# Performance work log

Hardware: AMD Instinct MI355X
Metric: run time of the kernel (lower is better)

The kernel has to match this reference:

```python
import jax, jax.numpy as jnp
import numpy as np

B, N, D, H, T, DFF, OUT = 32, 256, 512, 8, 60, 2048, 2
EPS = 1e-5


def _mha(q, k, v, Wq, Wk, Wv, Wo, bq, bk, bv, bo):
    # torch nn.MultiheadAttention (batch_first): x @ W.T + b projections
    Bq, Lq, Dm = q.shape
    dh = Dm // H
    scale = 1.0 / np.sqrt(dh).astype(np.float32)
    qh = (q @ Wq.T + bq).reshape(Bq, Lq, H, dh).transpose(0, 2, 1, 3)
    kh = (k @ Wk.T + bk).reshape(Bq, k.shape[1], H, dh).transpose(0, 2, 1, 3)
    vh = (v @ Wv.T + bv).reshape(Bq, v.shape[1], H, dh).transpose(0, 2, 1, 3)
    a = jax.nn.softmax(jnp.einsum('bhqd,bhkd->bhqk', qh, kh) * scale, axis=-1)
    o = jnp.einsum('bhqk,bhkd->bhqd', a, vh).transpose(0, 2, 1, 3).reshape(Bq, Lq, Dm)
    return o @ Wo.T + bo


def _ln(x, w, b):
    m = x.mean(-1, keepdims=True)
    v = ((x - m) ** 2).mean(-1, keepdims=True)
    return (x - m) / jnp.sqrt(v + EPS) * w + b


def setup_inputs() -> dict:
    key = jax.random.key(0)
    ks = iter(jax.random.split(key, 64))

    def rn(shape, s=0.05):
        return jax.random.normal(next(ks), shape, dtype=jnp.float32) * s

    inp = {
        'H_v_all': rn((B, N, D), 1.0),
        'H_v0_init': rn((B, 1, 1, D), 1.0),
        'pe': rn((1, T, D), 1.0),  # positional_encoding parameter
    }
    # s_* : spatial_attn;  sa_* : decoder self-attn;  ca_* : decoder cross-attn
    for p in ('s', 'sa', 'ca'):
        for m in ('Wq', 'Wk', 'Wv', 'Wo'):
            inp[f'{p}_{m}'] = rn((D, D))
        for m in ('bq', 'bk', 'bv', 'bo'):
            inp[f'{p}_{m}'] = jnp.zeros((D,), jnp.float32)
    for i in (1, 2, 3):
        inp[f'ln{i}_w'] = jnp.ones((D,), jnp.float32)
        inp[f'ln{i}_b'] = jnp.zeros((D,), jnp.float32)
    inp['W1'] = rn((DFF, D)); inp['b1'] = jnp.zeros((DFF,), jnp.float32)
    inp['W2'] = rn((D, DFF)); inp['b2'] = jnp.zeros((D,), jnp.float32)
    inp['Wout'] = rn((OUT, D)); inp['bout'] = jnp.zeros((OUT,), jnp.float32)
    return inp


def reference(H_v_all, H_v0_init, pe,
              s_Wq, s_Wk, s_Wv, s_Wo, s_bq, s_bk, s_bv, s_bo,
              sa_Wq, sa_Wk, sa_Wv, sa_Wo, sa_bq, sa_bk, sa_bv, sa_bo,
              ca_Wq, ca_Wk, ca_Wv, ca_Wo, ca_bq, ca_bk, ca_bv, ca_bo,
              ln1_w, ln1_b, ln2_w, ln2_b, ln3_w, ln3_b,
              W1, b1, W2, b2, Wout, bout):

    def dec_layer(x, mem):
        # post-norm TransformerDecoderLayer, no masks (non-causal), relu FFN, eval (no dropout)
        sa = _mha(x, x, x, sa_Wq, sa_Wk, sa_Wv, sa_Wo, sa_bq, sa_bk, sa_bv, sa_bo)
        x = _ln(x + sa, ln1_w, ln1_b)
        ca = _mha(x, mem, mem, ca_Wq, ca_Wk, ca_Wv, ca_Wo, ca_bq, ca_bk, ca_bv, ca_bo)
        x = _ln(x + ca, ln2_w, ln2_b)
        ff = jax.nn.relu(x @ W1.T + b1) @ W2.T + b2
        return _ln(x + ff, ln3_w, ln3_b)

    tgt = H_v0_init  # (B, 1, 1, D), grows along dim 2
    outputs = []
    for t in range(T):
        tgt_pe = tgt + pe[:, :t + 1][:, None]        # (B,1,t+1,D)
        tgt_step = tgt_pe.reshape(B, t + 1, D)
        ctx = _mha(tgt_step[:, -1:, :], H_v_all, H_v_all,
                   s_Wq, s_Wk, s_Wv, s_Wo, s_bq, s_bk, s_bv, s_bo)
        decoded = dec_layer(tgt_step, H_v_all)
        nxt = decoded[:, -1:, :] + ctx               # (B,1,D)
        tgt = jnp.concatenate([tgt, nxt[:, None]], axis=2)
        outputs.append(nxt[:, None])                 # (B,1,1,D)
    out_seq = jnp.concatenate(outputs, axis=2)       # (B,1,T,D)
    return out_seq @ Wout.T + bout                   # (B,1,T,2)
```

## Files before the change

kernel.cpp:

```cpp
#include <hip/hip_runtime.h>


#define NB 32
#define NN 256
#define DD 512
#define NH 8
#define DH 64
#define TT 60
#define DF 2048
#define NBLK 256
#define NTHR 512

typedef unsigned short ushort_t;
typedef _Float16 half2v __attribute__((ext_vector_type(2)));

constexpr size_t SZ_KV  = (size_t)NB * NN * DD;
constexpr size_t SZ_ROW = (size_t)NB * DD;
constexpr size_t SZ_PAR = (size_t)NB * NH * DD;
constexpr size_t OFF_KS32 = 0;
constexpr size_t OFF_VS32 = SZ_KV;
constexpr size_t OFF_KC32 = 2 * SZ_KV;
constexpr size_t OFF_VC32 = 3 * SZ_KV;
constexpr size_t OFF_X    = 0;
constexpr size_t OFF_U1P  = OFF_X   + SZ_ROW;
constexpr size_t OFF_U2P  = OFF_U1P + SZ_PAR;
constexpr size_t OFF_U3P  = OFF_U2P + SZ_PAR;
constexpr size_t OFF_CTP0 = OFF_U3P + SZ_PAR;
constexpr size_t OFF_CTP1 = OFF_CTP0 + SZ_PAR;
constexpr size_t OFF_BF   = 4 * SZ_KV;
constexpr size_t UOFF_KST = 0;
constexpr size_t UOFF_KCT = SZ_KV;
constexpr size_t UOFF_VSH = 2 * SZ_KV;
constexpr size_t UOFF_VCH = 3 * SZ_KV;
constexpr size_t UOFF_W8  = 4 * SZ_KV;
constexpr size_t UOFF_W1  = UOFF_W8 + 8ull * DD * DD;
constexpr size_t UOFF_W2  = UOFF_W1 + (size_t)DD * DF;
constexpr size_t UEND     = UOFF_W2 + (size_t)DF * DD;
constexpr size_t OFF_FLG  = OFF_BF + (UEND + 1) / 2;

constexpr unsigned DYN_LDS = 131072;

__device__ __forceinline__ float ldg_a(const float* p) {
  return __hip_atomic_load(p, __ATOMIC_RELAXED, __HIP_MEMORY_SCOPE_AGENT);
}
__device__ __forceinline__ void stg_a(float* p, float v) {
  __hip_atomic_store(p, v, __ATOMIC_RELAXED, __HIP_MEMORY_SCOPE_AGENT);
}
__device__ __forceinline__ unsigned f2pk(float a, float b) {
  return __builtin_bit_cast(unsigned, __builtin_amdgcn_cvt_pkrtz(a, b));
}
__device__ __forceinline__ ushort_t f2h(float a) {
  return (ushort_t)(f2pk(a, 0.f) & 0xffffu);
}
__device__ __forceinline__ float h2f(ushort_t u) {
  return (float)__builtin_bit_cast(_Float16, u);
}
__device__ __forceinline__ float fdot2u(unsigned a, unsigned b, float c) {
  return __builtin_amdgcn_fdot2(__builtin_bit_cast(half2v, a),
                                __builtin_bit_cast(half2v, b), c, false);
}

struct Params {
  const float *pe;
  const float *sa_bq, *sa_bk, *sa_bv, *s_bq, *sa_bo, *s_bo, *ca_bq, *ca_bo;
  const float *ln1w, *ln1b, *ln2w, *ln2b, *ln3w, *ln3b;
  const float *b1, *b2, *Wout, *bout;
  const ushort_t *w8, *w1b, *w2b;
  const ushort_t *KsT, *KcT, *VsH, *VcH;
  float *xcur, *u1p, *u2p, *u3p, *ctp0, *ctp1;
  float *out;
  unsigned *flags;
};

__device__ __forceinline__ void gbar(unsigned* fl, int tid, int h,
                                     unsigned& rnd) {
  __builtin_amdgcn_s_waitcnt(0);
  __syncthreads();
  rnd++;
  if (tid < 64) {
    if (tid == h)
      __hip_atomic_store(&fl[h], rnd, __ATOMIC_RELAXED,
                         __HIP_MEMORY_SCOPE_AGENT);
    bool wait = true;
    while (wait) {
      unsigned v = rnd;
      if (tid < 8)
        v = __hip_atomic_load(&fl[tid], __ATOMIC_RELAXED,
                              __HIP_MEMORY_SCOPE_AGENT);
      wait = __any(v < rnd);
    }
  }
  __syncthreads();
}

__global__ __launch_bounds__(512) void decode_persistent(Params P) {
  __shared__ __align__(16) float sX[2048];
  __shared__ __align__(16) float sPart[512];
  __shared__ float sAux[64];
  __shared__ __align__(16) unsigned xh[256];
  __shared__ __align__(16) unsigned ph[384];
  __shared__ __align__(16) ushort_t cacheK[TT * 78];
  __shared__ __align__(16) ushort_t cacheV[TT * 64];
  extern __shared__ __align__(16) unsigned dynLds[];
  unsigned* Ks_l = dynLds;
  unsigned* Kc_l = dynLds + 8192;
  ushort_t* Vs_l = (ushort_t*)(dynLds + 16384);
  ushort_t* Vc_l = Vs_l + 16384;

  int tid = threadIdx.x;
  int bid = blockIdx.x;
  int b = bid >> 3, h = bid & 7;
  int idx8 = bid;
  unsigned* fl = P.flags + b * 64;
  unsigned rnd = 0;

  {
    const uint4* gks = (const uint4*)((const unsigned*)P.KsT +
                       (((size_t)b * DD + h * DH) >> 1) * NN);
    const uint4* gkc = (const uint4*)((const unsigned*)P.KcT +
                       (((size_t)b * DD + h * DH) >> 1) * NN);
    const uint4* gvs = (const uint4*)(P.VsH + (size_t)idx8 * NN * DH);
    const uint4* gvc = (const uint4*)(P.VcH + (size_t)idx8 * NN * DH);
    uint4* dks = (uint4*)Ks_l;
    uint4* dkc = (uint4*)Kc_l;
    uint4* dvs = (uint4*)Vs_l;
    uint4* dvc = (uint4*)Vc_l;
    #pragma unroll
    for (int i = 0; i < 4; i++) {
      int idx = i * NTHR + tid;
      dks[idx] = gks[idx];
      dkc[idx] = gkc[idx];
      dvs[idx] = gvs[idx];
      dvc[idx] = gvc[idx];
    }
  }

  float x_f = ldg_a(P.xcur + (size_t)b * DD + tid);
  {
    float px = __shfl_xor(x_f, 1);
    if (!(tid & 1)) xh[tid >> 1] = f2pk(x_f, px);
  }
  __syncthreads();

  for (int t = 0; t < TT; t++) {
    {
      {
        int w = tid >> 6, c = tid & 63, m = w >> 1, half = w & 1;
        int col = h * DH + c;
        const uint2* wp = (const uint2*)(P.w8 + (size_t)m * DD * DD) + col;
        float acc = 0.f;
        #pragma unroll 8
        for (int kq = half * 64; kq < half * 64 + 64; kq++) {
          uint2 wv = wp[(size_t)kq * DD];
          uint2 xv = *(const uint2*)&xh[kq * 2];
          acc = fdot2u(wv.x, xv.x, acc);
          acc = fdot2u(wv.y, xv.y, acc);
        }
        sPart[tid] = acc;
      }
      __syncthreads();
      if (tid < 256) {
        int m = tid >> 6, c = tid & 63, col = h * DH + c;
        const float* bias = (m == 0) ? P.sa_bq : (m == 1) ? P.sa_bk
                          : (m == 2) ? P.sa_bv : P.s_bq;
        float val = sPart[(2 * m) * 64 + c] + sPart[(2 * m + 1) * 64 + c]
                    + bias[col];
        sX[512 + tid] = val;
        if (m == 1) cacheK[t * 78 + c] = f2h(val);
        if (m == 2) cacheV[t * 64 + c] = f2h(val);
      }
      __syncthreads();

      int L = t + 1;
      float* sQ  = sX + 512;
      float* sQs = sX + 704;
      float* sPb = sX + 768;
      if (tid < 64) {
        float e = 0.f;
        if (tid < L) {
          const unsigned* kl = (const unsigned*)(cacheK + (size_t)tid * 78);
          float a = 0.f;
          #pragma unroll 8
          for (int i = 0; i < 32; i++) {
            unsigned w = kl[i];
            a += sQ[2 * i] * h2f((ushort_t)(w & 0xffffu)) +
                 sQ[2 * i + 1] * h2f((ushort_t)(w >> 16));
          }
          e = __expf(a * 0.125f);
        }
        float s2 = e;
        #pragma unroll
        for (int s = 32; s >= 1; s >>= 1) s2 += __shfl_xor(s2, s);
        sPb[tid] = e * (1.f / s2);
        float o = 0.f;
        for (int j = 0; j < L; j++)
          o += sPb[j] * h2f(cacheV[j * 64 + tid]);
        float po = __shfl_xor(o, 1);
        if (!(tid & 1)) ph[32 + (tid >> 1)] = f2pk(o, po);
      } else if (tid < 320) {
        int n = tid - 64;
        float a = 0.f;
        #pragma unroll 8
        for (int i = 0; i < 32; i++) {
          unsigned w = Ks_l[i * NN + n];
          a += sQs[2 * i] * h2f((ushort_t)(w & 0xffffu)) +
               sQs[2 * i + 1] * h2f((ushort_t)(w >> 16));
        }
        sPart[n] = a * 0.125f;
      }
      __syncthreads();
      float* sPr = sX + 1536;
      if (tid < 256) {
        float e = __expf(sPart[tid]);
        sPr[tid] = e;
        int w = tid >> 6;
        float s2 = e;
        #pragma unroll
        for (int s = 32; s >= 1; s >>= 1) s2 += __shfl_xor(s2, s);
        if ((tid & 63) == 0) sAux[4 + w] = s2;
      }
      __syncthreads();
      float* sB = sX + 1024;
      {
        int g = tid >> 6, d = tid & 63;
        float inv = 1.f / (sAux[4] + sAux[5] + sAux[6] + sAux[7]);
        const ushort_t* vp = Vs_l + (g * 32) * DH + d;
        float acc = 0.f;
        #pragma unroll 4
        for (int n = 0; n < 32; n++) acc += sPr[g * 32 + n] * h2f(vp[n * DH]);
        sB[tid] = acc * inv;
      }
      __syncthreads();
      if (tid < 64) {
        float o = 0.f;
        #pragma unroll
        for (int i = 0; i < 8; i++) o += sB[i * 64 + tid];
        float po = __shfl_xor(o, 1);
        if (!(tid & 1)) ph[64 + (tid >> 1)] = f2pk(o, po);
      }
      __syncthreads();
      {
        float* ctp = ((t & 1) ? P.ctp1 : P.ctp0) + ((size_t)b * NH + h) * DD;
        float* u1p = P.u1p + ((size_t)b * NH + h) * DD;
        const uint2* wpa = (const uint2*)(P.w8 + 4ull * DD * DD) + tid;
        const uint2* wpb = (const uint2*)(P.w8 + 5ull * DD * DD) + tid;
        float acc1 = (h == 0) ? P.sa_bo[tid] + x_f : 0.f;
        float acc2 = (h == 0) ? P.s_bo[tid] : 0.f;
        #pragma unroll 8
        for (int j = 0; j < 16; j++) {
          int k4 = h * 16 + j;
          uint2 wv = wpa[(size_t)k4 * DD];
          uint2 x1 = *(const uint2*)&ph[32 + 2 * j];
          acc1 = fdot2u(wv.x, x1.x, acc1);
          acc1 = fdot2u(wv.y, x1.y, acc1);
          uint2 wv2 = wpb[(size_t)k4 * DD];
          uint2 x2 = *(const uint2*)&ph[64 + 2 * j];
          acc2 = fdot2u(wv2.x, x2.x, acc2);
          acc2 = fdot2u(wv2.y, x2.y, acc2);
        }
        stg_a(&u1p[tid], acc1);
        stg_a(&ctp[tid], acc2);
      }
    }
    gbar(fl, tid, h, rnd);

    float y1f;
    {
      float u = 0.f;
      {
        const float* pp = P.u1p + (size_t)b * NH * DD + tid;
        #pragma unroll
        for (int i = 0; i < 8; i++) u += ldg_a(pp + i * DD);
      }
      {
        int w = tid >> 6;
        float s = u, q2 = u * u;
        #pragma unroll
        for (int m = 32; m >= 1; m >>= 1) { s += __shfl_xor(s, m); q2 += __shfl_xor(q2, m); }
        if ((tid & 63) == 0) { sAux[w] = s; sAux[8 + w] = q2; }
      }
      __syncthreads();
      {
        float ss = 0.f, qq = 0.f;
        #pragma unroll
        for (int i = 0; i < 8; i++) { ss += sAux[i]; qq += sAux[8 + i]; }
        float mean = ss * (1.f / 512.f);
        float inv = rsqrtf(qq * (1.f / 512.f) - mean * mean + 1e-5f);
        y1f = (u - mean) * inv * P.ln1w[tid] + P.ln1b[tid];
        float py = __shfl_xor(y1f, 1);
        if (!(tid & 1)) ph[128 + (tid >> 1)] = f2pk(y1f, py);
      }
      __syncthreads();
      {
        int c = tid & 63, w = tid >> 6, col = h * DH + c;
        const uint2* wp = (const uint2*)(P.w8 + 6ull * DD * DD) + col;
        float acc = 0.f;
        #pragma unroll 8
        for (int kq = w * 16; kq < w * 16 + 16; kq++) {
          uint2 wv = wp[(size_t)kq * DD];
          uint2 xv = *(const uint2*)&ph[128 + 2 * kq];
          acc = fdot2u(wv.x, xv.x, acc);
          acc = fdot2u(wv.y, xv.y, acc);
        }
        sPart[tid] = acc;
      }
      __syncthreads();
      if (tid < 64) {
        float o = 0.f;
        #pragma unroll
        for (int i = 0; i < 8; i++) o += sPart[i * 64 + tid];
        o += P.ca_bq[h * DH + tid];
        float po = __shfl_xor(o, 1);
        if (!(tid & 1)) ph[tid >> 1] = f2pk(o, po);
      }
      __syncthreads();
      {
        int n = tid & 255, dh2 = tid >> 8;
        float a = 0.f;
        #pragma unroll 8
        for (int dw = dh2 * 16; dw < dh2 * 16 + 16; dw++)
          a = fdot2u(Kc_l[dw * NN + n], ph[dw], a);
        sPart[tid] = a;
      }
      __syncthreads();
      float* sPr = sX + 1536;
      if (tid < 256) {
        float e = __expf((sPart[tid] + sPart[256 + tid]) * 0.125f);
        sPr[tid] = e;
        int w = tid >> 6;
        float s2 = e;
        #pragma unroll
        for (int s = 32; s >= 1; s >>= 1) s2 += __shfl_xor(s2, s);
        if ((tid & 63) == 0) sAux[4 + w] = s2;
      }
      __syncthreads();
      float* sB = sX + 1024;
      {
        int g = tid >> 6, d = tid & 63;
        float inv = 1.f / (sAux[4] + sAux[5] + sAux[6] + sAux[7]);
        const ushort_t* vp = Vc_l + (g * 32) * DH + d;
        float acc = 0.f;
        #pragma unroll 4
        for (int n = 0; n < 32; n++) acc += sPr[g * 32 + n] * h2f(vp[n * DH]);
        sB[tid] = acc * inv;
      }
      __syncthreads();
      if (tid < 64) {
        float o = 0.f;
        #pragma unroll
        for (int i = 0; i < 8; i++) o += sB[i * 64 + tid];
        float po = __shfl_xor(o, 1);
        if (!(tid & 1)) ph[32 + (tid >> 1)] = f2pk(o, po);
      }
      __syncthreads();
      {
        const uint2* wp = (const uint2*)(P.w8 + 7ull * DD * DD) + tid;
        float acc = (h == 0) ? P.ca_bo[tid] + y1f : 0.f;
        #pragma unroll 8
        for (int j = 0; j < 16; j++) {
          int k4 = h * 16 + j;
          uint2 wv = wp[(size_t)k4 * DD];
          uint2 xv = *(const uint2*)&ph[32 + 2 * j];
          acc = fdot2u(wv.x, xv.x, acc);
          acc = fdot2u(wv.y, xv.y, acc);
        }
        stg_a(&P.u2p[((size_t)b * NH + h) * DD + tid], acc);
      }
    }
    gbar(fl, tid, h, rnd);

    float zf;
    {
      float v = 0.f;
      {
        const float* pp = P.u2p + (size_t)b * NH * DD + tid;
        #pragma unroll
        for (int i = 0; i < 8; i++) v += ldg_a(pp + i * DD);
      }
      {
        int w = tid >> 6;
        float s = v, q2 = v * v;
        #pragma unroll
        for (int m = 32; m >= 1; m >>= 1) { s += __shfl_xor(s, m); q2 += __shfl_xor(q2, m); }
        if ((tid & 63) == 0) { sAux[w] = s; sAux[8 + w] = q2; }
      }
      __syncthreads();
      {
        float ss = 0.f, qq = 0.f;
        #pragma unroll
        for (int i = 0; i < 8; i++) { ss += sAux[i]; qq += sAux[8 + i]; }
        float mean = ss * (1.f / 512.f);
        float inv = rsqrtf(qq * (1.f / 512.f) - mean * mean + 1e-5f);
        zf = (v - mean) * inv * P.ln2w[tid] + P.ln2b[tid];
        float pz = __shfl_xor(zf, 1);
        if (!(tid & 1)) ph[128 + (tid >> 1)] = f2pk(zf, pz);
      }
      __syncthreads();
      {
        int c = tid & 255, half = tid >> 8, col = h * 256 + c;
        const uint2* wp = (const uint2*)P.w1b + col;
        float acc = 0.f;
        #pragma unroll 8
        for (int kq = half * 64; kq < half * 64 + 64; kq++) {
          uint2 wv = wp[(size_t)kq * DF];
          uint2 xv = *(const uint2*)&ph[128 + 2 * kq];
          acc = fdot2u(wv.x, xv.x, acc);
          acc = fdot2u(wv.y, xv.y, acc);
        }
        sPart[tid] = acc;
      }
      __syncthreads();
      if (tid < 256) {
        float hv = fmaxf(sPart[tid] + sPart[256 + tid] + P.b1[h * 256 + tid], 0.f);
        float pv = __shfl_xor(hv, 1);
        if (!(tid & 1)) ph[tid >> 1] = f2pk(hv, pv);
      }
      __syncthreads();
      {
        const uint2* wp = (const uint2*)P.w2b + tid;
        float acc = (h == 0) ? zf + P.b2[tid] : 0.f;
        #pragma unroll 8
        for (int j = 0; j < 64; j++) {
          int k4 = h * 64 + j;
          uint2 wv = wp[(size_t)k4 * DD];
          uint2 xv = *(const uint2*)&ph[2 * j];
          acc = fdot2u(wv.x, xv.x, acc);
          acc = fdot2u(wv.y, xv.y, acc);
        }
        stg_a(&P.u3p[((size_t)b * NH + h) * DD + tid], acc);
      }
    }
    gbar(fl, tid, h, rnd);

    {
      float u = 0.f, ctxv = 0.f;
      {
        const float* pp = P.u3p + (size_t)b * NH * DD + tid;
        const float* cp = ((t & 1) ? P.ctp1 : P.ctp0) + (size_t)b * NH * DD + tid;
        #pragma unroll
        for (int i = 0; i < 8; i++) { u += ldg_a(pp + i * DD); ctxv += ldg_a(cp + i * DD); }
      }
      {
        int w = tid >> 6;
        float s = u, q2 = u * u;
        #pragma unroll
        for (int m = 32; m >= 1; m >>= 1) { s += __shfl_xor(s, m); q2 += __shfl_xor(q2, m); }
        if ((tid & 63) == 0) { sAux[w] = s; sAux[8 + w] = q2; }
      }
      __syncthreads();
      float ss = 0.f, qq = 0.f;
      #pragma unroll
      for (int i = 0; i < 8; i++) { ss += sAux[i]; qq += sAux[8 + i]; }
      float mean = ss * (1.f / 512.f);
      float inv = rsqrtf(qq * (1.f / 512.f) - mean * mean + 1e-5f);
      float nxt = (u - mean) * inv * P.ln3w[tid] + P.ln3b[tid] + ctxv;
      float p = (t < TT - 1) ? P.pe[(size_t)(t + 1) * DD + tid] : 0.f;
      x_f = nxt + p;
      {
        float px = __shfl_xor(x_f, 1);
        if (!(tid & 1)) xh[tid >> 1] = f2pk(x_f, px);
      }
      if (h == 0) sX[tid] = nxt;
      __syncthreads();
      if (h == 0) {
        {
          int c = tid >> 8, l = tid & 255;
          float a = sX[l] * P.Wout[(size_t)c * DD + l] +
                    sX[l + 256] * P.Wout[(size_t)c * DD + l + 256];
          #pragma unroll
          for (int m = 32; m >= 1; m >>= 1) a += __shfl_xor(a, m);
          if ((tid & 63) == 0) sAux[16 + (tid >> 6)] = a;
        }
        __syncthreads();
        if (tid == 0)
          P.out[((size_t)b * TT + t) * 2 + 0] =
              sAux[16] + sAux[17] + sAux[18] + sAux[19] + P.bout[0];
        if (tid == 256)
          P.out[((size_t)b * TT + t) * 2 + 1] =
              sAux[20] + sAux[21] + sAux[22] + sAux[23] + P.bout[1];
      }
      __syncthreads();
    }
  }
}

__global__ __launch_bounds__(256) void gemm_kv(
    const float* __restrict__ A,
    const float* __restrict__ W0, const float* __restrict__ W1_,
    const float* __restrict__ W2_, const float* __restrict__ W3_,
    const float* __restrict__ b0, const float* __restrict__ b1_,
    const float* __restrict__ b2_, const float* __restrict__ b3_,
    float* __restrict__ O0, float* __restrict__ O1,
    float* __restrict__ O2, float* __restrict__ O3) {
  __shared__ __align__(16) float As[8][128];
  __shared__ __align__(16) float Bs[8][128];
  int tid = threadIdx.x;
  int bx = blockIdx.x, by = blockIdx.y;
  int mm = bx >> 2;
  int col0 = (bx & 3) * 128;
  const float* W = mm == 0 ? W0 : mm == 1 ? W1_ : mm == 2 ? W2_ : W3_;
  const float* bias = mm == 0 ? b0 : mm == 1 ? b1_ : mm == 2 ? b2_ : b3_;
  float* O = mm == 0 ? O0 : mm == 1 ? O1 : mm == 2 ? O2 : O3;
  int tx = tid & 15, ty = tid >> 4;
  int m0 = by * 128;
  int lr = tid >> 1, lk = (tid & 1) * 4;
  const float* Ap = A + (size_t)(m0 + lr) * DD + lk;
  const float* Wp = W + (size_t)(col0 + lr) * DD + lk;
  float c[8][8] = {};
  for (int k0 = 0; k0 < DD; k0 += 8) {
    float4 av = *(const float4*)(Ap + k0);
    float4 wv = *(const float4*)(Wp + k0);
    __syncthreads();
    As[lk + 0][lr] = av.x; As[lk + 1][lr] = av.y; As[lk + 2][lr] = av.z; As[lk + 3][lr] = av.w;
    Bs[lk + 0][lr] = wv.x; Bs[lk + 1][lr] = wv.y; Bs[lk + 2][lr] = wv.z; Bs[lk + 3][lr] = wv.w;
    __syncthreads();
    #pragma unroll
    for (int k = 0; k < 8; k++) {
      float a[8], bb[8];
      *(float4*)&a[0] = *(const float4*)&As[k][ty * 8];
      *(float4*)&a[4] = *(const float4*)&As[k][ty * 8 + 4];
      *(float4*)&bb[0] = *(const float4*)&Bs[k][tx * 8];
      *(float4*)&bb[4] = *(const float4*)&Bs[k][tx * 8 + 4];
      #pragma unroll
      for (int i = 0; i < 8; i++)
        #pragma unroll
        for (int j = 0; j < 8; j++) c[i][j] += a[i] * bb[j];
    }
  }
  const float* bp = bias + col0 + tx * 8;
  for (int i = 0; i < 8; i++) {
    int row = m0 + ty * 8 + i;
    float* op = O + (size_t)row * DD + col0 + tx * 8;
    #pragma unroll
    for (int jq = 0; jq < 8; jq += 4) {
      float4 v;
      v.x = c[i][jq + 0] + bp[jq + 0];
      v.y = c[i][jq + 1] + bp[jq + 1];
      v.z = c[i][jq + 2] + bp[jq + 2];
      v.w = c[i][jq + 3] + bp[jq + 3];
      *(float4*)(op + jq) = v;
    }
  }
}

__global__ __launch_bounds__(256) void pack_kT(const float* __restrict__ Ks32,
                                               const float* __restrict__ Kc32,
                                               ushort_t* __restrict__ KsT,
                                               ushort_t* __restrict__ KcT) {
  int z = blockIdx.z;
  int b = z >> 1;
  const float* in = ((z & 1) ? Kc32 : Ks32) + (size_t)b * NN * DD;
  ushort_t* out = ((z & 1) ? KcT : KsT) + (size_t)b * NN * DD;
  int r0 = blockIdx.x * 32, c0 = blockIdx.y * 32;
  __shared__ float tile[32][33];
  int tid = threadIdx.x;
  int i = tid >> 3, j4 = (tid & 7) * 4;
  float4 v = *(const float4*)(in + (size_t)(r0 + i) * DD + c0 + j4);
  tile[i][j4] = v.x; tile[i][j4 + 1] = v.y; tile[i][j4 + 2] = v.z; tile[i][j4 + 3] = v.w;
  __syncthreads();
  int d = c0 + i;
  ushort_t* op = out + (size_t)(d >> 1) * (2 * NN) + 2 * (r0 + j4) + (d & 1);
  op[0] = f2h(tile[j4][i]);     op[2] = f2h(tile[j4 + 1][i]);
  op[4] = f2h(tile[j4 + 2][i]); op[6] = f2h(tile[j4 + 3][i]);
}

__global__ __launch_bounds__(256) void pack_vh(const float* __restrict__ Vs32,
                                               const float* __restrict__ Vc32,
                                               ushort_t* __restrict__ VsH,
                                               ushort_t* __restrict__ VcH) {
  const float* src = blockIdx.y ? Vc32 : Vs32;
  ushort_t* dst = blockIdx.y ? VcH : VsH;
  size_t idx = (size_t)blockIdx.x * 1024 + threadIdx.x * 4;
  float4 v = *(const float4*)(src + idx);
  int d512 = (int)(idx & 511);
  int n = (int)((idx >> 9) & 255);
  int b = (int)(idx >> 17);
  int h = d512 >> 6, d = d512 & 63;
  ushort_t* op = dst + (((size_t)(b * 8 + h) * NN + n) * DH + d);
  op[0] = f2h(v.x); op[1] = f2h(v.y); op[2] = f2h(v.z); op[3] = f2h(v.w);
}

struct PWItem { const float* in; ushort_t* out; int C; int K; };
struct PWArgs { PWItem m[10]; };
__global__ __launch_bounds__(256) void pack_w(PWArgs a) {
  PWItem it = a.m[blockIdx.y];
  int total = it.C * (it.K >> 2);
  int e = blockIdx.x * 256 + threadIdx.x;
  if (e >= total) return;
  int kd = it.K >> 2;
  int k4 = e % kd, col = e / kd;
  float4 v = *(const float4*)(it.in + (size_t)col * it.K + k4 * 4);
  unsigned lo = f2pk(v.x, v.y), hi = f2pk(v.z, v.w);
  ushort4 o;
  o.x = (ushort_t)(lo & 0xffffu); o.y = (ushort_t)(lo >> 16);
  o.z = (ushort_t)(hi & 0xffffu); o.w = (ushort_t)(hi >> 16);
  *((ushort4*)it.out + (size_t)k4 * it.C + col) = o;
}

__global__ __launch_bounds__(256) void init_x(const float* __restrict__ hv0,
                                              const float* __restrict__ pe,
                                              float* __restrict__ ws,
                                              unsigned* __restrict__ flags) {
  int i = blockIdx.x * 256 + threadIdx.x;
  ws[OFF_X + i] = hv0[i] + pe[i & (DD - 1)];
  if (i < 2048) flags[i] = 0u;
}

extern "C" void kernel_launch(void* const* d_in, const int* in_sizes, int n_in,
                              void* d_out, int out_size, void* d_ws, size_t ws_size,
                              hipStream_t stream) {
  const float* H_v_all = (const float*)d_in[0];
  const float* H_v0    = (const float*)d_in[1];
  const float* pe      = (const float*)d_in[2];
  const float* s_Wq = (const float*)d_in[3];
  const float* s_Wk = (const float*)d_in[4];
  const float* s_Wv = (const float*)d_in[5];
  const float* s_Wo = (const float*)d_in[6];
  const float* s_bq = (const float*)d_in[7];
  const float* s_bk = (const float*)d_in[8];
  const float* s_bv = (const float*)d_in[9];
  const float* s_bo = (const float*)d_in[10];
  const float* sa_Wq = (const float*)d_in[11];
  const float* sa_Wk = (const float*)d_in[12];
  const float* sa_Wv = (const float*)d_in[13];
  const float* sa_Wo = (const float*)d_in[14];
  const float* sa_bq = (const float*)d_in[15];
  const float* sa_bk = (const float*)d_in[16];
  const float* sa_bv = (const float*)d_in[17];
  const float* sa_bo = (const float*)d_in[18];
  const float* ca_Wq = (const float*)d_in[19];
  const float* ca_Wk = (const float*)d_in[20];
  const float* ca_Wv = (const float*)d_in[21];
  const float* ca_Wo = (const float*)d_in[22];
  const float* ca_bq = (const float*)d_in[23];
  const float* ca_bk = (const float*)d_in[24];
  const float* ca_bv = (const float*)d_in[25];
  const float* ca_bo = (const float*)d_in[26];
  const float* ln1w = (const float*)d_in[27];
  const float* ln1b = (const float*)d_in[28];
  const float* ln2w = (const float*)d_in[29];
  const float* ln2b = (const float*)d_in[30];
  const float* ln3w = (const float*)d_in[31];
  const float* ln3b = (const float*)d_in[32];
  const float* W1   = (const float*)d_in[33];
  const float* b1   = (const float*)d_in[34];
  const float* W2   = (const float*)d_in[35];
  const float* b2   = (const float*)d_in[36];
  const float* Wout = (const float*)d_in[37];
  const float* bout = (const float*)d_in[38];

  float* ws = (float*)d_ws;
  float* Ks32 = ws + OFF_KS32;
  float* Vs32 = ws + OFF_VS32;
  float* Kc32 = ws + OFF_KC32;
  float* Vc32 = ws + OFF_VC32;
  ushort_t* ub = (ushort_t*)(ws + OFF_BF);
  unsigned* flags = (unsigned*)(ws + OFF_FLG);

  hipLaunchKernelGGL(gemm_kv, dim3(16, 64), dim3(256), 0, stream,
                     H_v_all, s_Wk, s_Wv, ca_Wk, ca_Wv,
                     s_bk, s_bv, ca_bk, ca_bv, Ks32, Vs32, Kc32, Vc32);

  hipLaunchKernelGGL(pack_kT, dim3(8, 16, 64), dim3(256), 0, stream,
                     Ks32, Kc32, ub + UOFF_KST, ub + UOFF_KCT);
  hipLaunchKernelGGL(pack_vh, dim3((unsigned)(SZ_KV / 1024), 2), dim3(256), 0,
                     stream, Vs32, Vc32, ub + UOFF_VSH, ub + UOFF_VCH);

  PWArgs pw;
  pw.m[0] = {sa_Wq, ub + UOFF_W8 + 0ull * DD * DD, DD, DD};
  pw.m[1] = {sa_Wk, ub + UOFF_W8 + 1ull * DD * DD, DD, DD};
  pw.m[2] = {sa_Wv, ub + UOFF_W8 + 2ull * DD * DD, DD, DD};
  pw.m[3] = {s_Wq,  ub + UOFF_W8 + 3ull * DD * DD, DD, DD};
  pw.m[4] = {sa_Wo, ub + UOFF_W8 + 4ull * DD * DD, DD, DD};
  pw.m[5] = {s_Wo,  ub + UOFF_W8 + 5ull * DD * DD, DD, DD};
  pw.m[6] = {ca_Wq, ub + UOFF_W8 + 6ull * DD * DD, DD, DD};
  pw.m[7] = {ca_Wo, ub + UOFF_W8 + 7ull * DD * DD, DD, DD};
  pw.m[8] = {W1, ub + UOFF_W1, DF, DD};
  pw.m[9] = {W2, ub + UOFF_W2, DD, DF};
  hipLaunchKernelGGL(pack_w, dim3(1024, 10), dim3(256), 0, stream, pw);

  hipLaunchKernelGGL(init_x, dim3(64), dim3(256), 0, stream,
                     H_v0, pe, ws, flags);

  static bool attr_set = false;
  if (!attr_set) {
    hipFuncSetAttribute((const void*)decode_persistent,
                        hipFuncAttributeMaxDynamicSharedMemorySize, DYN_LDS);
    attr_set = true;
  }

  Params P;
  P.pe = pe;
  P.sa_bq = sa_bq; P.sa_bk = sa_bk; P.sa_bv = sa_bv; P.s_bq = s_bq;
  P.sa_bo = sa_bo; P.s_bo = s_bo; P.ca_bq = ca_bq; P.ca_bo = ca_bo;
  P.ln1w = ln1w; P.ln1b = ln1b; P.ln2w = ln2w; P.ln2b = ln2b;
  P.ln3w = ln3w; P.ln3b = ln3b;
  P.b1 = b1; P.b2 = b2; P.Wout = Wout; P.bout = bout;
  P.w8 = ub + UOFF_W8; P.w1b = ub + UOFF_W1; P.w2b = ub + UOFF_W2;
  P.KsT = ub + UOFF_KST; P.KcT = ub + UOFF_KCT;
  P.VsH = ub + UOFF_VSH; P.VcH = ub + UOFF_VCH;
  P.xcur = ws + OFF_X;
  P.u1p = ws + OFF_U1P; P.u2p = ws + OFF_U2P; P.u3p = ws + OFF_U3P;
  P.ctp0 = ws + OFF_CTP0; P.ctp1 = ws + OFF_CTP1;
  P.out = (float*)d_out;
  P.flags = flags;

  void* kargs[] = { (void*)&P };
  hipLaunchCooperativeKernel((void*)decode_persistent, dim3(NBLK), dim3(NTHR),
                             kargs, DYN_LDS, stream);
}
```

Baseline: 2.173 ms.

## Split group barrier into flag set/wait and publish self-attn output early

Replaces the combined group barrier with separate set_flag and wait_ge primitives that use monotonically increasing per-step target values. The self-attention output projection now runs and signals before the spatial-attention softmax and context projection, so the cross-group wait overlaps with that remaining work. This is meant to cut the idle time at each inter-block barrier in the persistent decode loop. It relies on the ctx buffers being double-buffered by t parity so later reads still see completed data, and it adds more ordering subtlety to the flag protocol.

```diff
diff --git a/kernel.cpp b/kernel.cpp
--- a/kernel.cpp
+++ b/kernel.cpp
@@ -72,22 +72,24 @@
   unsigned *flags;
 };
 
-__device__ __forceinline__ void gbar(unsigned* fl, int tid, int h,
-                                     unsigned& rnd) {
+__device__ __forceinline__ void set_flag(unsigned* fl, int tid, int h,
+                                         unsigned val) {
   __builtin_amdgcn_s_waitcnt(0);
   __syncthreads();
-  rnd++;
+  if (tid == 0)
+    __hip_atomic_store(&fl[h], val, __ATOMIC_RELAXED,
+                       __HIP_MEMORY_SCOPE_AGENT);
+}
+__device__ __forceinline__ void wait_ge(unsigned* fl, int tid,
+                                        unsigned target) {
   if (tid < 64) {
-    if (tid == h)
-      __hip_atomic_store(&fl[h], rnd, __ATOMIC_RELAXED,
-                         __HIP_MEMORY_SCOPE_AGENT);
     bool wait = true;
     while (wait) {
-      unsigned v = rnd;
+      unsigned v = target;
       if (tid < 8)
         v = __hip_atomic_load(&fl[tid], __ATOMIC_RELAXED,
                               __HIP_MEMORY_SCOPE_AGENT);
-      wait = __any(v < rnd);
+      wait = __any(v < target);
     }
   }
   __syncthreads();
@@ -209,6 +211,21 @@
         sPart[n] = a * 0.125f;
       }
       __syncthreads();
+      {
+        float* u1p = P.u1p + ((size_t)b * NH + h) * DD;
+        const uint2* wpa = (const uint2*)(P.w8 + 4ull * DD * DD) + tid;
+        float acc1 = (h == 0) ? P.sa_bo[tid] + x_f : 0.f;
+        #pragma unroll 8
+        for (int j = 0; j < 16; j++) {
+          int k4 = h * 16 + j;
+          uint2 wv = wpa[(size_t)k4 * DD];
+          uint2 x1 = *(const uint2*)&ph[32 + 2 * j];
+          acc1 = fdot2u(wv.x, x1.x, acc1);
+          acc1 = fdot2u(wv.y, x1.y, acc1);
+        }
+        stg_a(&u1p[tid], acc1);
+      }
+      set_flag(fl, tid, h, 3 * t + 1);
       float* sPr = sX + 1536;
       if (tid < 256) {
         float e = __expf(sPart[tid]);
@@ -241,31 +258,23 @@
       __syncthreads();
       {
         float* ctp = ((t & 1) ? P.ctp1 : P.ctp0) + ((size_t)b * NH + h) * DD;
-        float* u1p = P.u1p + ((size_t)b * NH + h) * DD;
-        const uint2* wpa = (const uint2*)(P.w8 + 4ull * DD * DD) + tid;
         const uint2* wpb = (const uint2*)(P.w8 + 5ull * DD * DD) + tid;
-        float acc1 = (h == 0) ? P.sa_bo[tid] + x_f : 0.f;
         float acc2 = (h == 0) ? P.s_bo[tid] : 0.f;
         #pragma unroll 8
         for (int j = 0; j < 16; j++) {
           int k4 = h * 16 + j;
-          uint2 wv = wpa[(size_t)k4 * DD];
-          uint2 x1 = *(const uint2*)&ph[32 + 2 * j];
-          acc1 = fdot2u(wv.x, x1.x, acc1);
-          acc1 = fdot2u(wv.y, x1.y, acc1);
           uint2 wv2 = wpb[(size_t)k4 * DD];
           uint2 x2 = *(const uint2*)&ph[64 + 2 * j];
           acc2 = fdot2u(wv2.x, x2.x, acc2);
           acc2 = fdot2u(wv2.y, x2.y, acc2);
         }
-        stg_a(&u1p[tid], acc1);
         stg_a(&ctp[tid], acc2);
       }
     }
-    gbar(fl, tid, h, rnd);
 
     float y1f;
     {
+      wait_ge(fl, tid, 3 * t + 1);
       float u = 0.f;
       {
         const float* pp = P.u1p + (size_t)b * NH * DD + tid;
@@ -367,10 +376,11 @@
         stg_a(&P.u2p[((size_t)b * NH + h) * DD + tid], acc);
       }
     }
-    gbar(fl, tid, h, rnd);
+    set_flag(fl, tid, h, 3 * t + 2);
 
     float zf;
     {
+      wait_ge(fl, tid, 3 * t + 2);
       float v = 0.f;
       {
         const float* pp = P.u2p + (size_t)b * NH * DD + tid;
@@ -430,9 +440,10 @@
         stg_a(&P.u3p[((size_t)b * NH + h) * DD + tid], acc);
       }
     }
-    gbar(fl, tid, h, rnd);
+    set_flag(fl, tid, h, 3 * t + 3);
 
     {
+      wait_ge(fl, tid, 3 * t + 3);
       float u = 0.f, ctxv = 0.f;
       {
         const float* pp = P.u3p + (size_t)b * NH * DD + tid;
@@ -482,6 +493,7 @@
       __syncthreads();
     }
   }
+  (void)rnd;
 }
 
 __global__ __launch_bounds__(256) void gemm_kv(
```

After: 2.082 ms. 4.2% less time.
